# Kernel tuning notes

Measured on AMD Instinct MI355X. Metric: run time of the kernel, lower is better.

Reference implementation:

```python
import jax, jax.numpy as jnp
import numpy as np

B, S, D, E, K = 4, 4096, 2048, 64, 2
H = D // 2  # router hidden dim
LN_EPS = 1e-5


def setup_inputs() -> dict:
    key = jax.random.key(0)
    kx, k1, k2 = jax.random.split(key, 3)
    # Xavier-uniform-ish scales for the two linears
    s1 = float(np.sqrt(6.0 / (D + H)))
    s2 = float(np.sqrt(6.0 / (H + E)))
    return {
        "x": jax.random.normal(kx, (B, S, D), dtype=jnp.float32),
        "W1": jax.random.uniform(k1, (D, H), jnp.float32, -s1, s1),
        "b1": jnp.zeros((H,), jnp.float32),
        "gamma": jnp.ones((H,), jnp.float32),
        "beta": jnp.zeros((H,), jnp.float32),
        "W2": jax.random.uniform(k2, (H, E), jnp.float32, -s2, s2),
        "b2": jnp.zeros((E,), jnp.float32),
    }


def reference(x, W1, b1, gamma, beta, W2, b2):
    # x: [B,S,D] -> flatten tokens
    xf = x.reshape(-1, D)                       # [N, D]
    h = xf @ W1 + b1                            # [N, H]
    mu = jnp.mean(h, axis=-1, keepdims=True)
    var = jnp.var(h, axis=-1, keepdims=True)
    h = (h - mu) * jax.lax.rsqrt(var + LN_EPS) * gamma + beta
    h = jax.nn.gelu(h, approximate=False)       # torch nn.GELU default = exact erf
    logits = h @ W2 + b2                        # [N, E]
    probs = jax.nn.softmax(logits, axis=-1)
    w, idx = jax.lax.top_k(probs, K)            # [N, K]
    w = w / (jnp.sum(w, axis=-1, keepdims=True) + 1e-9)
    idx = idx.reshape(B, S, K)
    w = w.reshape(B, S, K)
    return idx, w, logits
```

## Files before the change

kernel.cpp:

```cpp
#include <hip/hip_runtime.h>
#include <hip/hip_bf16.h>
#include <cmath>

#define N_TOK 16384
#define D_DIM 2048
#define H_DIM 1024
#define E_DIM 64

typedef _Float16 half8 __attribute__((ext_vector_type(8)));
typedef float floatx4 __attribute__((ext_vector_type(4)));

#define GLOAD_LDS(gp, lp)                                                      \
  __builtin_amdgcn_global_load_lds(                                            \
      (const __attribute__((address_space(1))) unsigned int*)(gp),             \
      (__attribute__((address_space(3))) unsigned int*)(lp), 16, 0, 0)

__global__ __launch_bounds__(256) void splitT_w1_kernel(
    const float* __restrict__ W1, _Float16* __restrict__ whT,
    _Float16* __restrict__ wlT) {
  __shared__ float ls[64][65];
  const int k0 = blockIdx.x * 64;
  const int c0 = blockIdx.y * 64;
  const int t = threadIdx.x;
  const int tr = t >> 6;
  const int tc = t & 63;
#pragma unroll
  for (int i = 0; i < 16; i++) {
    int k = tr * 16 + i;
    ls[k][tc] = W1[(size_t)(k0 + k) * H_DIM + c0 + tc];
  }
  __syncthreads();
#pragma unroll
  for (int i = 0; i < 16; i++) {
    int c = tr * 16 + i;
    float v = ls[tc][c];
    _Float16 hv = (_Float16)v;
    _Float16 lv = (_Float16)(v - (float)hv);
    whT[(size_t)(c0 + c) * D_DIM + k0 + tc] = hv;
    wlT[(size_t)(c0 + c) * D_DIM + k0 + tc] = lv;
  }
}

__global__ __launch_bounds__(256) void pack_w2_kernel(
    const float* __restrict__ W2, _Float16* __restrict__ pW2h,
    _Float16* __restrict__ pW2l) {
  const int s = blockIdx.x;
  const int ng = threadIdx.x >> 6;
  const int lane = threadIdx.x & 63;
  const int kg = lane >> 4, fr = lane & 15;
  half8 hh, ll;
#pragma unroll
  for (int j = 0; j < 8; j++) {
    const float v = W2[(size_t)(s * 32 + kg * 8 + j) * E_DIM + ng * 16 + fr];
    const _Float16 hv = (_Float16)v;
    hh[j] = hv;
    ll[j] = (_Float16)(v - (float)hv);
  }
  const size_t idx = (((size_t)s * 4 + ng) * 64 + lane) * 8;
  *(half8*)(pW2h + idx) = hh;
  *(half8*)(pW2l + idx) = ll;
}

__global__ __launch_bounds__(512, 2) void gemm1_mfma_kernel(
    const float* __restrict__ x, const _Float16* __restrict__ whT,
    const _Float16* __restrict__ wlT, float* __restrict__ h) {
  extern __shared__ __align__(16) char smem[];

  const int t = threadIdx.x;
  const int wave = t >> 6;
  const int lane = t & 63;

  const int bid = blockIdx.x;
  const int swz = (bid & 7) * 32 + (bid >> 3);
  const int by = swz >> 2, bx = swz & 3;
  const int row0 = by * 256, col0 = bx * 256;
  const int wr = wave >> 2, wc = wave & 3;

  floatx4 acc[8][4];
#pragma unroll
  for (int m = 0; m < 8; m++)
#pragma unroll
    for (int n = 0; n < 4; n++) acc[m][n] = (floatx4){0.f, 0.f, 0.f, 0.f};

  int awaddr[2];
  size_t gaoff[2];
#pragma unroll
  for (int q = 0; q < 2; q++) {
    const int u = q * 512 + t;
    const int arow = u >> 2;
    const int aslot = u & 3;
    awaddr[q] = arow * 64 + ((aslot ^ ((arow >> 1) & 3)) << 4);
    gaoff[q] = (size_t)(row0 + arow) * D_DIM + aslot * 8;
  }

  int ldsoff[2];
  size_t gboff[2];
#pragma unroll
  for (int q = 0; q < 2; q++) {
    const int o = q * 8192 + t * 16;
    const int row = o >> 6;
    const int ss = ((o >> 4) & 3) ^ ((row >> 1) & 3);
    ldsoff[q] = q * 8192 + wave * 1024;
    gboff[q] = (size_t)(col0 + row) * D_DIM + ss * 8;
  }

  const int kg = lane >> 4;
  const int fr = lane & 15;

  int afr[8], bfr[4];
#pragma unroll
  for (int m = 0; m < 8; m++) {
    const int r = wr * 128 + m * 16 + fr;
    afr[m] = r * 64 + ((kg ^ ((r >> 1) & 3)) << 4);
  }
#pragma unroll
  for (int n = 0; n < 4; n++) {
    const int c = wc * 64 + n * 16 + fr;
    bfr[n] = c * 64 + ((kg ^ ((c >> 1) & 3)) << 4);
  }

  float4 av[2][2];

#define LOAD_A(T)                                                              \
  do {                                                                         \
    const size_t kk = (size_t)(T) * 32;                                        \
    av[0][0] = *(const float4*)(x + gaoff[0] + kk);                            \
    av[0][1] = *(const float4*)(x + gaoff[0] + kk + 4);                        \
    av[1][0] = *(const float4*)(x + gaoff[1] + kk);                            \
    av[1][1] = *(const float4*)(x + gaoff[1] + kk + 4);                        \
  } while (0)

#define WRITE_A(B)                                                             \
  do {                                                                         \
    char* lb = smem + (B) * 65536;                                             \
    _Pragma("unroll") for (int q = 0; q < 2; q++) {                            \
      float vs[8] = {av[q][0].x, av[q][0].y, av[q][0].z, av[q][0].w,           \
                     av[q][1].x, av[q][1].y, av[q][1].z, av[q][1].w};          \
      half8 hh, ll;                                                            \
      _Pragma("unroll") for (int j = 0; j < 8; j++) {                          \
        _Float16 hv = (_Float16)vs[j];                                         \
        hh[j] = hv;                                                            \
        ll[j] = (_Float16)(vs[j] - (float)hv);                                 \
      }                                                                        \
      *(half8*)(lb + awaddr[q]) = hh;                                          \
      *(half8*)(lb + 16384 + awaddr[q]) = ll;                                  \
    }                                                                          \
  } while (0)

#define GLD_B(T)                                                               \
  do {                                                                         \
    const size_t kk = (size_t)(T) * 32;                                        \
    char* db = smem + ((T) & 1) * 65536;                                       \
    GLOAD_LDS(whT + gboff[0] + kk, db + 32768 + ldsoff[0]);                    \
    GLOAD_LDS(whT + gboff[1] + kk, db + 32768 + ldsoff[1]);                    \
    GLOAD_LDS(wlT + gboff[0] + kk, db + 49152 + ldsoff[0]);                    \
    GLOAD_LDS(wlT + gboff[1] + kk, db + 49152 + ldsoff[1]);                    \
  } while (0)

#define BODY(T, STG)                                                           \
  do {                                                                         \
    const char* cb = smem + ((T) & 1) * 65536;                                 \
    if ((STG) < 2) GLD_B((T) + 1);                                             \
    __builtin_amdgcn_sched_barrier(0);                                         \
    half8 bh[4], bl[4];                                                        \
    _Pragma("unroll") for (int n = 0; n < 4; n++) {                            \
      bh[n] = *(const half8*)(cb + 32768 + bfr[n]);                            \
      bl[n] = *(const half8*)(cb + 49152 + bfr[n]);                            \
    }                                                                          \
    _Pragma("unroll") for (int m = 0; m < 8; m++) {                            \
      half8 ah = *(const half8*)(cb + afr[m]);                                 \
      half8 al = *(const half8*)(cb + 16384 + afr[m]);                         \
      __builtin_amdgcn_s_setprio(1);                                           \
      _Pragma("unroll") for (int n = 0; n < 4; n++) {                          \
        acc[m][n] = __builtin_amdgcn_mfma_f32_16x16x32_f16(ah, bh[n],          \
                                                           acc[m][n], 0, 0, 0);\
        acc[m][n] = __builtin_amdgcn_mfma_f32_16x16x32_f16(ah, bl[n],          \
                                                           acc[m][n], 0, 0, 0);\
        acc[m][n] = __builtin_amdgcn_mfma_f32_16x16x32_f16(al, bh[n],          \
                                                           acc[m][n], 0, 0, 0);\
      }                                                                        \
      __builtin_amdgcn_s_setprio(0);                                           \
    }                                                                          \
    __builtin_amdgcn_sched_barrier(0);                                         \
    if ((STG) < 2) {                                                           \
      WRITE_A(((T) + 1) & 1);                                                  \
      if ((STG) == 0) {                                                        \
        LOAD_A((T) + 2);                                                       \
        __builtin_amdgcn_sched_barrier(0);                                     \
        asm volatile("s_waitcnt vmcnt(4)" ::: "memory");                       \
      } else {                                                                 \
        __builtin_amdgcn_sched_barrier(0);                                     \
        asm volatile("s_waitcnt vmcnt(0)" ::: "memory");                       \
      }                                                                        \
      asm volatile("s_waitcnt lgkmcnt(0)" ::: "memory");                       \
      __builtin_amdgcn_s_barrier();                                            \
      __builtin_amdgcn_sched_barrier(0);                                       \
    }                                                                          \
  } while (0)

  LOAD_A(0);
  GLD_B(0);
  WRITE_A(0);
  LOAD_A(1);
  asm volatile("s_waitcnt vmcnt(4)" ::: "memory");
  asm volatile("s_waitcnt lgkmcnt(0)" ::: "memory");
  __builtin_amdgcn_s_barrier();
  __builtin_amdgcn_sched_barrier(0);

#pragma unroll 1
  for (int T = 0; T < 62; ++T) {
    BODY(T, 0);
  }
  BODY(62, 1);
  BODY(63, 2);

#undef LOAD_A
#undef WRITE_A
#undef GLD_B
#undef BODY

  const int rj = (lane >> 4) * 4;
#pragma unroll
  for (int m = 0; m < 8; m++) {
    const int rbase = row0 + wr * 128 + m * 16 + rj;
#pragma unroll
    for (int n = 0; n < 4; n++) {
      const int c = col0 + wc * 64 + n * 16 + fr;
#pragma unroll
      for (int j = 0; j < 4; j++) {
        h[(size_t)(rbase + j) * H_DIM + c] = acc[m][n][j];
      }
    }
  }
}

__device__ __forceinline__ float gelu_exact(float v) {
  return 0.5f * v * (1.0f + erff(v * 0.70710678118654752f));
}

__global__ __launch_bounds__(256) void router_kernel(
    const float* __restrict__ hbuf, const float* __restrict__ b1,
    const float* __restrict__ gamma, const float* __restrict__ beta,
    const _Float16* __restrict__ pW2h, const _Float16* __restrict__ pW2l,
    const float* __restrict__ b2, float* __restrict__ out) {
  extern __shared__ __align__(16) char rsm[];
  char* gh = rsm;
  char* gl = rsm + 32768;
  float* lg = (float*)(rsm + 65536);

  const int t = threadIdx.x;
  const int tok0 = blockIdx.x * 16;

  const int tk = t >> 4;
  const int l16 = t & 15;
  {
    const float* hr = hbuf + (size_t)(tok0 + tk) * H_DIM;
    float vals[64];
    float s = 0.f, s2 = 0.f;
#pragma unroll
    for (int q2 = 0; q2 < 8; q2++) {
      const int j = q2 * 128 + l16 * 8;
      float4 v0 = *(const float4*)(hr + j);
      float4 v1 = *(const float4*)(hr + j + 4);
      float4 b0 = *(const float4*)(b1 + j);
      float4 b1v = *(const float4*)(b1 + j + 4);
      v0.x += b0.x; v0.y += b0.y; v0.z += b0.z; v0.w += b0.w;
      v1.x += b1v.x; v1.y += b1v.y; v1.z += b1v.z; v1.w += b1v.w;
      vals[q2 * 8 + 0] = v0.x; vals[q2 * 8 + 1] = v0.y;
      vals[q2 * 8 + 2] = v0.z; vals[q2 * 8 + 3] = v0.w;
      vals[q2 * 8 + 4] = v1.x; vals[q2 * 8 + 5] = v1.y;
      vals[q2 * 8 + 6] = v1.z; vals[q2 * 8 + 7] = v1.w;
      s += v0.x + v0.y + v0.z + v0.w + v1.x + v1.y + v1.z + v1.w;
      s2 += v0.x * v0.x + v0.y * v0.y + v0.z * v0.z + v0.w * v0.w +
            v1.x * v1.x + v1.y * v1.y + v1.z * v1.z + v1.w * v1.w;
    }
#pragma unroll
    for (int off = 8; off; off >>= 1) {
      s += __shfl_xor(s, off, 16);
      s2 += __shfl_xor(s2, off, 16);
    }
    const float mean = s * (1.f / 1024.f);
    const float var = s2 * (1.f / 1024.f) - mean * mean;
    const float rstd = rsqrtf(var + 1e-5f);
    const int swz = ((tk >> 1) & 3);
#pragma unroll
    for (int q2 = 0; q2 < 8; q2++) {
      const int j = q2 * 128 + l16 * 8;
      half8 hh, ll;
#pragma unroll
      for (int e = 0; e < 8; e++) {
        const int jj = q2 * 8 + e;
        const int col = j + e;
        const float gm = gamma[col], bt = beta[col];
        const float gv = gelu_exact((vals[jj] - mean) * rstd * gm + bt);
        const _Float16 hv = (_Float16)gv;
        hh[e] = hv;
        ll[e] = (_Float16)(gv - (float)hv);
      }
      const int sidx = q2 * 4 + (l16 >> 2);
      const int addr = sidx * 1024 + tk * 64 + (((l16 & 3) ^ swz) << 4);
      *(half8*)(gh + addr) = hh;
      *(half8*)(gl + addr) = ll;
    }
  }
  __syncthreads();

  const int wave = t >> 6;
  const int lane = t & 63;
  const int kg = lane >> 4;
  const int fr = lane & 15;
  {
    floatx4 acc = (floatx4){0.f, 0.f, 0.f, 0.f};
    const int aswz = ((fr >> 1) & 3);
#pragma unroll
    for (int s = 0; s < 32; s++) {
      const int aaddr = s * 1024 + fr * 64 + ((kg ^ aswz) << 4);
      half8 ah = *(const half8*)(gh + aaddr);
      half8 al = *(const half8*)(gl + aaddr);
      const size_t bo = (((size_t)s * 4 + wave) * 64 + lane) * 8;
      half8 bh = *(const half8*)(pW2h + bo);
      half8 bl = *(const half8*)(pW2l + bo);
      acc = __builtin_amdgcn_mfma_f32_16x16x32_f16(ah, bh, acc, 0, 0, 0);
      acc = __builtin_amdgcn_mfma_f32_16x16x32_f16(ah, bl, acc, 0, 0, 0);
      acc = __builtin_amdgcn_mfma_f32_16x16x32_f16(al, bh, acc, 0, 0, 0);
    }
#pragma unroll
    for (int j = 0; j < 4; j++) {
      lg[(kg * 4 + j) * E_DIM + wave * 16 + fr] = acc[j];
    }
  }
  __syncthreads();

  float* out_idx = out;
  float* out_w = out + 32768;
  float* out_logits = out + 65536;

  const float b2v = b2[lane];
#pragma unroll
  for (int tt = 0; tt < 4; tt++) {
    const int tok = wave * 4 + tt;
    const int n = tok0 + tok;
    const float L = lg[tok * E_DIM + lane] + b2v;
    float m = L;
#pragma unroll
    for (int off = 32; off; off >>= 1) m = fmaxf(m, __shfl_xor(m, off));
    const float ex = expf(L - m);
    float sum = ex;
#pragma unroll
    for (int off = 32; off; off >>= 1) sum += __shfl_xor(sum, off);

    float v1 = L; int i1 = lane;
#pragma unroll
    for (int off = 32; off; off >>= 1) {
      float ov = __shfl_xor(v1, off);
      int oi = __shfl_xor(i1, off);
      if (ov > v1 || (ov == v1 && oi < i1)) { v1 = ov; i1 = oi; }
    }
    float v2 = (lane == i1) ? -1e30f : L; int i2 = lane;
#pragma unroll
    for (int off = 32; off; off >>= 1) {
      float ov = __shfl_xor(v2, off);
      int oi = __shfl_xor(i2, off);
      if (ov > v2 || (ov == v2 && oi < i2)) { v2 = ov; i2 = oi; }
    }

    out_logits[(size_t)n * 64 + lane] = L;
    if (lane == 0) {
      const float p1 = expf(v1 - m) / sum;
      const float p2 = expf(v2 - m) / sum;
      const float dn = p1 + p2 + 1e-9f;
      out_idx[n * 2 + 0] = (float)i1;
      out_idx[n * 2 + 1] = (float)i2;
      out_w[n * 2 + 0] = p1 / dn;
      out_w[n * 2 + 1] = p2 / dn;
    }
  }
}

extern "C" void kernel_launch(void* const* d_in, const int* in_sizes, int n_in,
                              void* d_out, int out_size, void* d_ws, size_t ws_size,
                              hipStream_t stream) {
  const float* x = (const float*)d_in[0];
  const float* W1 = (const float*)d_in[1];
  const float* b1 = (const float*)d_in[2];
  const float* gamma = (const float*)d_in[3];
  const float* beta = (const float*)d_in[4];
  const float* W2 = (const float*)d_in[5];
  const float* b2 = (const float*)d_in[6];
  float* out = (float*)d_out;

  char* ws = (char*)d_ws;
  _Float16* whT = (_Float16*)ws;
  _Float16* wlT = (_Float16*)(ws + 4194304);
  float* hbuf = (float*)(ws + 8388608);
  _Float16* pW2h = (_Float16*)(ws + 75497472);
  _Float16* pW2l = (_Float16*)(ws + 75628544);

  (void)hipFuncSetAttribute((const void*)gemm1_mfma_kernel,
                            hipFuncAttributeMaxDynamicSharedMemorySize,
                            131072);
  (void)hipFuncSetAttribute((const void*)router_kernel,
                            hipFuncAttributeMaxDynamicSharedMemorySize,
                            69632);

  splitT_w1_kernel<<<dim3(D_DIM / 64, H_DIM / 64), 256, 0, stream>>>(W1, whT, wlT);
  pack_w2_kernel<<<32, 256, 0, stream>>>(W2, pW2h, pW2l);

  gemm1_mfma_kernel<<<256, 512, 131072, stream>>>(x, whT, wlT, hbuf);

  router_kernel<<<N_TOK / 16, 256, 69632, stream>>>(hbuf, b1, gamma, beta,
                                                    pW2h, pW2l, b2, out);
}
```

Measured before the change: 263.9 us.

## Split GEMM K-step into four phases interleaving loads with MFMA

Restructures the main GEMM loop body into four phases. Each phase loads B fragments and two A fragments from LDS, issues one memory stage (B-hi global-to-LDS, B-lo, A write to LDS, next A global load), then runs 24 MFMAs, with block barriers around each phase. The aim is to spread memory traffic across the compute so LDS and global loads overlap MFMA work instead of clustering before or after it. In exchange it adds more s_barriers per iteration and reloads the B fragments in every phase, which raises LDS read traffic and synchronisation overhead.

```diff
diff --git a/kernel.cpp b/kernel.cpp
--- a/kernel.cpp
+++ b/kernel.cpp
@@ -147,59 +147,124 @@
     }                                                                          \
   } while (0)
 
-#define GLD_B(T)                                                               \
+#define GLD_B_HI(T)                                                            \
   do {                                                                         \
     const size_t kk = (size_t)(T) * 32;                                        \
     char* db = smem + ((T) & 1) * 65536;                                       \
     GLOAD_LDS(whT + gboff[0] + kk, db + 32768 + ldsoff[0]);                    \
     GLOAD_LDS(whT + gboff[1] + kk, db + 32768 + ldsoff[1]);                    \
+  } while (0)
+
+#define GLD_B_LO(T)                                                            \
+  do {                                                                         \
+    const size_t kk = (size_t)(T) * 32;                                        \
+    char* db = smem + ((T) & 1) * 65536;                                       \
     GLOAD_LDS(wlT + gboff[0] + kk, db + 49152 + ldsoff[0]);                    \
     GLOAD_LDS(wlT + gboff[1] + kk, db + 49152 + ldsoff[1]);                    \
   } while (0)
 
+#define PHASE(P, STAGE, END)                                                   \
+  do {                                                                         \
+    half8 bh0 = *(const half8*)(cb + 32768 + bfr[0]);                          \
+    half8 bl0 = *(const half8*)(cb + 49152 + bfr[0]);                          \
+    half8 bh1 = *(const half8*)(cb + 32768 + bfr[1]);                          \
+    half8 bl1 = *(const half8*)(cb + 49152 + bfr[1]);                          \
+    half8 bh2 = *(const half8*)(cb + 32768 + bfr[2]);                          \
+    half8 bl2 = *(const half8*)(cb + 49152 + bfr[2]);                          \
+    half8 bh3 = *(const half8*)(cb + 32768 + bfr[3]);                          \
+    half8 bl3 = *(const half8*)(cb + 49152 + bfr[3]);                          \
+    half8 ah0 = *(const half8*)(cb + afr[2 * (P)]);                            \
+    half8 al0 = *(const half8*)(cb + 16384 + afr[2 * (P)]);                    \
+    half8 ah1 = *(const half8*)(cb + afr[2 * (P) + 1]);                        \
+    half8 al1 = *(const half8*)(cb + 16384 + afr[2 * (P) + 1]);                \
+    STAGE;                                                                     \
+    __builtin_amdgcn_sched_barrier(0);                                         \
+    __builtin_amdgcn_s_barrier();                                              \
+    asm volatile("s_waitcnt lgkmcnt(0)" ::: "memory");                         \
+    __builtin_amdgcn_sched_barrier(0);                                         \
+    __builtin_amdgcn_s_setprio(1);                                             \
+    acc[2 * (P)][0] = __builtin_amdgcn_mfma_f32_16x16x32_f16(                  \
+        ah0, bh0, acc[2 * (P)][0], 0, 0, 0);                                   \
+    acc[2 * (P)][0] = __builtin_amdgcn_mfma_f32_16x16x32_f16(                  \
+        ah0, bl0, acc[2 * (P)][0], 0, 0, 0);                                   \
+    acc[2 * (P)][0] = __builtin_amdgcn_mfma_f32_16x16x32_f16(                  \
+        al0, bh0, acc[2 * (P)][0], 0, 0, 0);                                   \
+    acc[2 * (P)][1] = __builtin_amdgcn_mfma_f32_16x16x32_f16(                  \
+        ah0, bh1, acc[2 * (P)][1], 0, 0, 0);                                   \
+    acc[2 * (P)][1] = __builtin_amdgcn_mfma_f32_16x16x32_f16(                  \
+        ah0, bl1, acc[2 * (P)][1], 0, 0, 0);                                   \
+    acc[2 * (P)][1] = __builtin_amdgcn_mfma_f32_16x16x32_f16(                  \
+        al0, bh1, acc[2 * (P)][1], 0, 0, 0);                                   \
+    acc[2 * (P)][2] = __builtin_amdgcn_mfma_f32_16x16x32_f16(                  \
+        ah0, bh2, acc[2 * (P)][2], 0, 0, 0);                                   \
+    acc[2 * (P)][2] = __builtin_amdgcn_mfma_f32_16x16x32_f16(                  \
+        ah0, bl2, acc[2 * (P)][2], 0, 0, 0);                                   \
+    acc[2 * (P)][2] = __builtin_amdgcn_mfma_f32_16x16x32_f16(                  \
+        al0, bh2, acc[2 * (P)][2], 0, 0, 0);                                   \
+    acc[2 * (P)][3] = __builtin_amdgcn_mfma_f32_16x16x32_f16(                  \
+        ah0, bh3, acc[2 * (P)][3], 0, 0, 0);                                   \
+    acc[2 * (P)][3] = __builtin_amdgcn_mfma_f32_16x16x32_f16(                  \
+        ah0, bl3, acc[2 * (P)][3], 0, 0, 0);                                   \
+    acc[2 * (P)][3] = __builtin_amdgcn_mfma_f32_16x16x32_f16(                  \
+        al0, bh3, acc[2 * (P)][3], 0, 0, 0);                                   \
+    acc[2 * (P) + 1][0] = __builtin_amdgcn_mfma_f32_16x16x32_f16(              \
+        ah1, bh0, acc[2 * (P) + 1][0], 0, 0, 0);                               \
+    acc[2 * (P) + 1][0] = __builtin_amdgcn_mfma_f32_16x16x32_f16(              \
+        ah1, bl0, acc[2 * (P) + 1][0], 0, 0, 0);                               \
+    acc[2 * (P) + 1][0] = __builtin_amdgcn_mfma_f32_16x16x32_f16(              \
+        al1, bh0, acc[2 * (P) + 1][0], 0, 0, 0);                               \
+    acc[2 * (P) + 1][1] = __builtin_amdgcn_mfma_f32_16x16x32_f16(              \
+        ah1, bh1, acc[2 * (P) + 1][1], 0, 0, 0);                               \
+    acc[2 * (P) + 1][1] = __builtin_amdgcn_mfma_f32_16x16x32_f16(              \
+        ah1, bl1, acc[2 * (P) + 1][1], 0, 0, 0);                               \
+    acc[2 * (P) + 1][1] = __builtin_amdgcn_mfma_f32_16x16x32_f16(              \
+        al1, bh1, acc[2 * (P) + 1][1], 0, 0, 0);                               \
+    acc[2 * (P) + 1][2] = __builtin_amdgcn_mfma_f32_16x16x32_f16(              \
+        ah1, bh2, acc[2 * (P) + 1][2], 0, 0, 0);                               \
+    acc[2 * (P) + 1][2] = __builtin_amdgcn_mfma_f32_16x16x32_f16(              \
+        ah1, bl2, acc[2 * (P) + 1][2], 0, 0, 0);                               \
+    acc[2 * (P) + 1][2] = __builtin_amdgcn_mfma_f32_16x16x32_f16(              \
+        al1, bh2, acc[2 * (P) + 1][2], 0, 0, 0);                               \
+    acc[2 * (P) + 1][3] = __builtin_amdgcn_mfma_f32_16x16x32_f16(              \
+        ah1, bh3, acc[2 * (P) + 1][3], 0, 0, 0);                               \
+    acc[2 * (P) + 1][3] = __builtin_amdgcn_mfma_f32_16x16x32_f16(              \
+        ah1, bl3, acc[2 * (P) + 1][3], 0, 0, 0);                               \
+    acc[2 * (P) + 1][3] = __builtin_amdgcn_mfma_f32_16x16x32_f16(              \
+        al1, bh3, acc[2 * (P) + 1][3], 0, 0, 0);                               \
+    __builtin_amdgcn_s_setprio(0);                                             \
+    __builtin_amdgcn_sched_barrier(0);                                         \
+    END;                                                                       \
+    __builtin_amdgcn_s_barrier();                                              \
+    __builtin_amdgcn_sched_barrier(0);                                         \
+  } while (0)
+
+#define NOP_STAGE do { } while (0)
+
 #define BODY(T, STG)                                                           \
   do {                                                                         \
     const char* cb = smem + ((T) & 1) * 65536;                                 \
-    if ((STG) < 2) GLD_B((T) + 1);                                             \
-    __builtin_amdgcn_sched_barrier(0);                                         \
-    half8 bh[4], bl[4];                                                        \
-    _Pragma("unroll") for (int n = 0; n < 4; n++) {                            \
-      bh[n] = *(const half8*)(cb + 32768 + bfr[n]);                            \
-      bl[n] = *(const half8*)(cb + 49152 + bfr[n]);                            \
+    if ((STG) < 2) {                                                           \
+      PHASE(0, GLD_B_HI((T) + 1), NOP_STAGE);                                  \
+      PHASE(1, GLD_B_LO((T) + 1), NOP_STAGE);                                  \
+      PHASE(2, WRITE_A(((T) + 1) & 1), NOP_STAGE);                             \
+      if ((STG) == 0) {                                                        \
+        PHASE(3, LOAD_A((T) + 2),                                              \
+              asm volatile("s_waitcnt vmcnt(4)" ::: "memory"));                \
+      } else {                                                                 \
+        PHASE(3, NOP_STAGE,                                                    \
+              asm volatile("s_waitcnt vmcnt(0)" ::: "memory"));                \
+      }                                                                        \
+    } else {                                                                   \
+      PHASE(0, NOP_STAGE, NOP_STAGE);                                          \
+      PHASE(1, NOP_STAGE, NOP_STAGE);                                          \
+      PHASE(2, NOP_STAGE, NOP_STAGE);                                          \
+      PHASE(3, NOP_STAGE, NOP_STAGE);                                          \
     }                                                                          \
-    _Pragma("unroll") for (int m = 0; m < 8; m++) {                            \
-      half8 ah = *(const half8*)(cb + afr[m]);                                 \
-      half8 al = *(const half8*)(cb + 16384 + afr[m]);                         \
-      __builtin_amdgcn_s_setprio(1);                                           \
-      _Pragma("unroll") for (int n = 0; n < 4; n++) {                          \
-        acc[m][n] = __builtin_amdgcn_mfma_f32_16x16x32_f16(ah, bh[n],          \
-                                                           acc[m][n], 0, 0, 0);\
-        acc[m][n] = __builtin_amdgcn_mfma_f32_16x16x32_f16(ah, bl[n],          \
-                                                           acc[m][n], 0, 0, 0);\
-        acc[m][n] = __builtin_amdgcn_mfma_f32_16x16x32_f16(al, bh[n],          \
-                                                           acc[m][n], 0, 0, 0);\
-      }                                                                        \
-      __builtin_amdgcn_s_setprio(0);                                           \
-    }                                                                          \
-    __builtin_amdgcn_sched_barrier(0);                                         \
-    if ((STG) < 2) {                                                           \
-      WRITE_A(((T) + 1) & 1);                                                  \
-      if ((STG) == 0) {                                                        \
-        LOAD_A((T) + 2);                                                       \
-        __builtin_amdgcn_sched_barrier(0);                                     \
-        asm volatile("s_waitcnt vmcnt(4)" ::: "memory");                       \
-      } else {                                                                 \
-        __builtin_amdgcn_sched_barrier(0);                                     \
-        asm volatile("s_waitcnt vmcnt(0)" ::: "memory");                       \
-      }                                                                        \
-      asm volatile("s_waitcnt lgkmcnt(0)" ::: "memory");                       \
-      __builtin_amdgcn_s_barrier();                                            \
-      __builtin_amdgcn_sched_barrier(0);                                       \
-    }                                                                          \
   } while (0)
 
   LOAD_A(0);
-  GLD_B(0);
+  GLD_B_HI(0);
+  GLD_B_LO(0);
   WRITE_A(0);
   LOAD_A(1);
   asm volatile("s_waitcnt vmcnt(4)" ::: "memory");
@@ -216,7 +281,10 @@
 
 #undef LOAD_A
 #undef WRITE_A
-#undef GLD_B
+#undef GLD_B_HI
+#undef GLD_B_LO
+#undef PHASE
+#undef NOP_STAGE
 #undef BODY
 
   const int rj = (lane >> 4) * 4;
```

Result: slower. 289.4 us (+9.7%).

## Split GEMM1 tile across 16 waves with 1024-thread blocks

Applied to the files above, without the earlier changes.

Doubles the workgroup to 1024 threads so each of 16 waves computes a 64x64 sub-tile instead of 128x64. Per-thread accumulators, A loads and B global-to-LDS copies are halved, and the vmcnt waits are adjusted to match. The aim is more waves to hide LDS and memory latency at the same 256x256 block tile. The cost is that each B fragment loaded from LDS is reused across fewer MFMAs, adding LDS traffic per FLOP. There are also more waves to synchronise at each barrier, and the 128KB LDS buffer still allows only one block per CU.

```diff
diff --git a/kernel.cpp b/kernel.cpp
--- a/kernel.cpp
+++ b/kernel.cpp
@@ -61,7 +61,7 @@
   *(half8*)(pW2l + idx) = ll;
 }
 
-__global__ __launch_bounds__(512, 2) void gemm1_mfma_kernel(
+__global__ __launch_bounds__(1024, 4) void gemm1_mfma_kernel(
     const float* __restrict__ x, const _Float16* __restrict__ whT,
     const _Float16* __restrict__ wlT, float* __restrict__ h) {
   extern __shared__ __align__(16) char smem[];
@@ -76,41 +76,30 @@
   const int row0 = by * 256, col0 = bx * 256;
   const int wr = wave >> 2, wc = wave & 3;
 
-  floatx4 acc[8][4];
-#pragma unroll
-  for (int m = 0; m < 8; m++)
+  floatx4 acc[4][4];
+#pragma unroll
+  for (int m = 0; m < 4; m++)
 #pragma unroll
     for (int n = 0; n < 4; n++) acc[m][n] = (floatx4){0.f, 0.f, 0.f, 0.f};
 
-  int awaddr[2];
-  size_t gaoff[2];
-#pragma unroll
-  for (int q = 0; q < 2; q++) {
-    const int u = q * 512 + t;
-    const int arow = u >> 2;
-    const int aslot = u & 3;
-    awaddr[q] = arow * 64 + ((aslot ^ ((arow >> 1) & 3)) << 4);
-    gaoff[q] = (size_t)(row0 + arow) * D_DIM + aslot * 8;
-  }
-
-  int ldsoff[2];
-  size_t gboff[2];
-#pragma unroll
-  for (int q = 0; q < 2; q++) {
-    const int o = q * 8192 + t * 16;
-    const int row = o >> 6;
-    const int ss = ((o >> 4) & 3) ^ ((row >> 1) & 3);
-    ldsoff[q] = q * 8192 + wave * 1024;
-    gboff[q] = (size_t)(col0 + row) * D_DIM + ss * 8;
-  }
+  const int arow = t >> 2;
+  const int aslot = t & 3;
+  const int awaddr = arow * 64 + ((aslot ^ ((arow >> 1) & 3)) << 4);
+  const size_t gaoff = (size_t)(row0 + arow) * D_DIM + aslot * 8;
+
+  const int bo_ = t * 16;
+  const int brow = bo_ >> 6;
+  const int bss = ((bo_ >> 4) & 3) ^ ((brow >> 1) & 3);
+  const int ldsBoff = wave * 1024;
+  const size_t gboff = (size_t)(col0 + brow) * D_DIM + bss * 8;
 
   const int kg = lane >> 4;
   const int fr = lane & 15;
 
-  int afr[8], bfr[4];
-#pragma unroll
-  for (int m = 0; m < 8; m++) {
-    const int r = wr * 128 + m * 16 + fr;
+  int afr[4], bfr[4];
+#pragma unroll
+  for (int m = 0; m < 4; m++) {
+    const int r = wr * 64 + m * 16 + fr;
     afr[m] = r * 64 + ((kg ^ ((r >> 1) & 3)) << 4);
   }
 #pragma unroll
@@ -119,42 +108,35 @@
     bfr[n] = c * 64 + ((kg ^ ((c >> 1) & 3)) << 4);
   }
 
-  float4 av[2][2];
+  float4 av0, av1;
 
 #define LOAD_A(T)                                                              \
   do {                                                                         \
-    const size_t kk = (size_t)(T) * 32;                                        \
-    av[0][0] = *(const float4*)(x + gaoff[0] + kk);                            \
-    av[0][1] = *(const float4*)(x + gaoff[0] + kk + 4);                        \
-    av[1][0] = *(const float4*)(x + gaoff[1] + kk);                            \
-    av[1][1] = *(const float4*)(x + gaoff[1] + kk + 4);                        \
+    const float* pa = x + gaoff + (size_t)(T) * 32;                            \
+    av0 = *(const float4*)pa;                                                  \
+    av1 = *(const float4*)(pa + 4);                                            \
   } while (0)
 
 #define WRITE_A(B)                                                             \
   do {                                                                         \
     char* lb = smem + (B) * 65536;                                             \
-    _Pragma("unroll") for (int q = 0; q < 2; q++) {                            \
-      float vs[8] = {av[q][0].x, av[q][0].y, av[q][0].z, av[q][0].w,           \
-                     av[q][1].x, av[q][1].y, av[q][1].z, av[q][1].w};          \
-      half8 hh, ll;                                                            \
-      _Pragma("unroll") for (int j = 0; j < 8; j++) {                          \
-        _Float16 hv = (_Float16)vs[j];                                         \
-        hh[j] = hv;                                                            \
-        ll[j] = (_Float16)(vs[j] - (float)hv);                                 \
-      }                                                                        \
-      *(half8*)(lb + awaddr[q]) = hh;                                          \
-      *(half8*)(lb + 16384 + awaddr[q]) = ll;                                  \
+    float vs[8] = {av0.x, av0.y, av0.z, av0.w, av1.x, av1.y, av1.z, av1.w};    \
+    half8 hh, ll;                                                              \
+    _Pragma("unroll") for (int j = 0; j < 8; j++) {                            \
+      _Float16 hv = (_Float16)vs[j];                                           \
+      hh[j] = hv;                                                              \
+      ll[j] = (_Float16)(vs[j] - (float)hv);                                   \
     }                                                                          \
+    *(half8*)(lb + awaddr) = hh;                                               \
+    *(half8*)(lb + 16384 + awaddr) = ll;                                       \
   } while (0)
 
 #define GLD_B(T)                                                               \
   do {                                                                         \
     const size_t kk = (size_t)(T) * 32;                                        \
     char* db = smem + ((T) & 1) * 65536;                                       \
-    GLOAD_LDS(whT + gboff[0] + kk, db + 32768 + ldsoff[0]);                    \
-    GLOAD_LDS(whT + gboff[1] + kk, db + 32768 + ldsoff[1]);                    \
-    GLOAD_LDS(wlT + gboff[0] + kk, db + 49152 + ldsoff[0]);                    \
-    GLOAD_LDS(wlT + gboff[1] + kk, db + 49152 + ldsoff[1]);                    \
+    GLOAD_LDS(whT + gboff + kk, db + 32768 + ldsBoff);                         \
+    GLOAD_LDS(wlT + gboff + kk, db + 49152 + ldsBoff);                         \
   } while (0)
 
 #define BODY(T, STG)                                                           \
@@ -167,7 +149,7 @@
       bh[n] = *(const half8*)(cb + 32768 + bfr[n]);                            \
       bl[n] = *(const half8*)(cb + 49152 + bfr[n]);                            \
     }                                                                          \
-    _Pragma("unroll") for (int m = 0; m < 8; m++) {                            \
+    _Pragma("unroll") for (int m = 0; m < 4; m++) {                            \
       half8 ah = *(const half8*)(cb + afr[m]);                                 \
       half8 al = *(const half8*)(cb + 16384 + afr[m]);                         \
       __builtin_amdgcn_s_setprio(1);                                           \
@@ -183,11 +165,11 @@
     }                                                                          \
     __builtin_amdgcn_sched_barrier(0);                                         \
     if ((STG) < 2) {                                                           \
-      WRITE_A(((T) + 1) & 1);                                                  \
+      WRITE_A(((T) + 1) & 1);      \
       if ((STG) == 0) {                                                        \
         LOAD_A((T) + 2);                                                       \
         __builtin_amdgcn_sched_barrier(0);                                     \
-        asm volatile("s_waitcnt vmcnt(4)" ::: "memory");                       \
+        asm volatile("s_waitcnt vmcnt(2)" ::: "memory");    \
       } else {                                                                 \
         __builtin_amdgcn_sched_barrier(0);                                     \
         asm volatile("s_waitcnt vmcnt(0)" ::: "memory");                       \
@@ -202,7 +184,7 @@
   GLD_B(0);
   WRITE_A(0);
   LOAD_A(1);
-  asm volatile("s_waitcnt vmcnt(4)" ::: "memory");
+  asm volatile("s_waitcnt vmcnt(2)" ::: "memory");
   asm volatile("s_waitcnt lgkmcnt(0)" ::: "memory");
   __builtin_amdgcn_s_barrier();
   __builtin_amdgcn_sched_barrier(0);
@@ -221,8 +203,8 @@
 
   const int rj = (lane >> 4) * 4;
 #pragma unroll
-  for (int m = 0; m < 8; m++) {
-    const int rbase = row0 + wr * 128 + m * 16 + rj;
+  for (int m = 0; m < 4; m++) {
+    const int rbase = row0 + wr * 64 + m * 16 + rj;
 #pragma unroll
     for (int n = 0; n < 4; n++) {
       const int c = col0 + wc * 64 + n * 16 + fr;
@@ -406,7 +388,7 @@
   splitT_w1_kernel<<<dim3(D_DIM / 64, H_DIM / 64), 256, 0, stream>>>(W1, whT, wlT);
   pack_w2_kernel<<<32, 256, 0, stream>>>(W2, pW2h, pW2l);
 
-  gemm1_mfma_kernel<<<256, 512, 131072, stream>>>(x, whT, wlT, hbuf);
+  gemm1_mfma_kernel<<<256, 1024, 131072, stream>>>(x, whT, wlT, hbuf);
 
   router_kernel<<<N_TOK / 16, 256, 69632, stream>>>(hbuf, b1, gamma, beta,
                                                     pW2h, pW2l, b2, out);
```

Result: no change. 265.6 us (+0.6%).
